# Performance work log

Hardware: AMD Instinct MI355X
Metric: run time of the kernel (lower is better)

## Reference

```python
import jax, jax.numpy as jnp
import numpy as np

DETA = 0.2  # constant margin scale (args.deta_const == True)
N = 33554432


def setup_inputs() -> dict:
    key = jax.random.key(0)
    k1, k2 = jax.random.split(key)
    y_pred = jax.random.normal(k1, (N,), dtype=jnp.float32)
    labels = jax.random.randint(k2, (N,), 0, 2, dtype=jnp.int32)
    return {"y_pred": y_pred, "labels": labels}


def reference(y_pred, labels):
    # Flattened ranking loss: deta * sum_{i in neg, j in pos} (neg_i - pos_j) / (pos_num * neg_num)
    # Algebraically: pos_num * sum(neg) - neg_num * sum(pos), avoiding the O(P*N) pairwise matrix.
    y = y_pred.reshape(-1)
    lab = labels.reshape(-1).astype(y.dtype)
    n_total = jnp.asarray(y.shape[0], dtype=y.dtype)
    pos_num = jnp.sum(lab)
    neg_num = n_total - pos_num
    sum_all = jnp.sum(y)
    sum_pos = jnp.sum(y * lab)
    sum_neg = sum_all - sum_pos
    valid = (pos_num > 0) & (neg_num > 0)
    denom = jnp.where(valid, pos_num * neg_num, jnp.ones_like(pos_num))
    loss = DETA * (pos_num * sum_neg - neg_num * sum_pos) / denom
    return jnp.where(valid, loss, jnp.zeros_like(loss))
```

## Files before the change

kernel.cpp:

```cpp
#include <hip/hip_runtime.h>


#define NBLK 2048

__global__ void aux_loss_reduce(const float* __restrict__ y,
                                const int* __restrict__ lab,
                                double* __restrict__ part, int n) {
    const int n4 = n >> 2;
    const float4* __restrict__ y4 = (const float4*)y;
    const int4* __restrict__ l4 = (const int4*)lab;

    double s_all = 0.0, s_pos = 0.0;
    int cnt = 0;

    const int idx = blockIdx.x * blockDim.x + threadIdx.x;
    const int stride = gridDim.x * blockDim.x;

    int i = idx;
    for (; i + stride < n4; i += 2 * stride) {
        float4 va = y4[i];
        int4 la = l4[i];
        float4 vb = y4[i + stride];
        int4 lb = l4[i + stride];

        s_all += (double)va.x + (double)va.y + (double)va.z + (double)va.w;
        s_pos += (la.x ? (double)va.x : 0.0) + (la.y ? (double)va.y : 0.0)
               + (la.z ? (double)va.z : 0.0) + (la.w ? (double)va.w : 0.0);
        cnt += la.x + la.y + la.z + la.w;

        s_all += (double)vb.x + (double)vb.y + (double)vb.z + (double)vb.w;
        s_pos += (lb.x ? (double)vb.x : 0.0) + (lb.y ? (double)vb.y : 0.0)
               + (lb.z ? (double)vb.z : 0.0) + (lb.w ? (double)vb.w : 0.0);
        cnt += lb.x + lb.y + lb.z + lb.w;
    }
    for (; i < n4; i += stride) {
        float4 v = y4[i];
        int4 l = l4[i];
        s_all += (double)v.x + (double)v.y + (double)v.z + (double)v.w;
        s_pos += (l.x ? (double)v.x : 0.0) + (l.y ? (double)v.y : 0.0)
               + (l.z ? (double)v.z : 0.0) + (l.w ? (double)v.w : 0.0);
        cnt += l.x + l.y + l.z + l.w;
    }
    for (int j = (n4 << 2) + idx; j < n; j += stride) {
        float v = y[j];
        int l = lab[j];
        s_all += (double)v;
        if (l) { s_pos += (double)v; cnt += l; }
    }

    double c = (double)cnt;

    for (int off = 32; off > 0; off >>= 1) {
        s_all += __shfl_down(s_all, off);
        s_pos += __shfl_down(s_pos, off);
        c     += __shfl_down(c, off);
    }

    __shared__ double sh_all[4], sh_pos[4], sh_cnt[4];
    const int wave = threadIdx.x >> 6;
    const int lane = threadIdx.x & 63;
    if (lane == 0) { sh_all[wave] = s_all; sh_pos[wave] = s_pos; sh_cnt[wave] = c; }
    __syncthreads();

    if (threadIdx.x == 0) {
        double a = 0.0, p = 0.0, cc = 0.0;
        for (int w = 0; w < 4; ++w) { a += sh_all[w]; p += sh_pos[w]; cc += sh_cnt[w]; }
        part[blockIdx.x]            = a;
        part[NBLK + blockIdx.x]     = p;
        part[2 * NBLK + blockIdx.x] = cc;
    }
}

__global__ void aux_loss_stage2(const double* __restrict__ part,
                                float* __restrict__ out, double n_total) {
    double a = 0.0, p = 0.0, cc = 0.0;
    for (int i = threadIdx.x; i < NBLK; i += blockDim.x) {
        a  += part[i];
        p  += part[NBLK + i];
        cc += part[2 * NBLK + i];
    }
    for (int off = 32; off > 0; off >>= 1) {
        a  += __shfl_down(a, off);
        p  += __shfl_down(p, off);
        cc += __shfl_down(cc, off);
    }
    __shared__ double sh_a[4], sh_p[4], sh_c[4];
    const int wave = threadIdx.x >> 6;
    const int lane = threadIdx.x & 63;
    if (lane == 0) { sh_a[wave] = a; sh_p[wave] = p; sh_c[wave] = cc; }
    __syncthreads();

    if (threadIdx.x == 0) {
        double sum_all = 0.0, sum_pos = 0.0, pos = 0.0;
        for (int w = 0; w < 4; ++w) { sum_all += sh_a[w]; sum_pos += sh_p[w]; pos += sh_c[w]; }
        double neg = n_total - pos;
        double sum_neg = sum_all - sum_pos;
        double loss = 0.0;
        if (pos > 0.0 && neg > 0.0) {
            loss = 0.2 * (pos * sum_neg - neg * sum_pos) / (pos * neg);
        }
        out[0] = (float)loss;
    }
}

extern "C" void kernel_launch(void* const* d_in, const int* in_sizes, int n_in,
                              void* d_out, int out_size, void* d_ws, size_t ws_size,
                              hipStream_t stream) {
    const float* y = (const float*)d_in[0];
    const int* lab = (const int*)d_in[1];
    int n = in_sizes[0];

    double* part = (double*)d_ws;

    aux_loss_reduce<<<NBLK, 256, 0, stream>>>(y, lab, part, n);
    aux_loss_stage2<<<1, 256, 0, stream>>>(part, (float*)d_out, (double)n);
}
```

Measured before the change: 274.9 us.

## Accumulate partial sums in FP32 per unrolled chunk and use contiguous per-block ranges

Each thread now sums 16 elements in float and only promotes to double once per chunk, replacing per-element double conversions and adds. The grid-stride loop becomes a contiguous per-block range with 4 independent vector loads in flight per thread, plus launch bounds. This aims to remove FP64 ALU cost that dominated the memory-bound reduction, at a small cost in accumulation precision.

```diff
diff --git a/kernel.cpp b/kernel.cpp
--- a/kernel.cpp
+++ b/kernel.cpp
@@ -2,50 +2,58 @@
 
 
 #define NBLK 2048
+#define TPB 256
+#define UNROLL 4
 
-__global__ void aux_loss_reduce(const float* __restrict__ y,
-                                const int* __restrict__ lab,
-                                double* __restrict__ part, int n) {
+__global__ __launch_bounds__(TPB, 8)
+void aux_loss_reduce(const float* __restrict__ y,
+                     const int* __restrict__ lab,
+                     double* __restrict__ part, int n) {
     const int n4 = n >> 2;
     const float4* __restrict__ y4 = (const float4*)y;
     const int4* __restrict__ l4 = (const int4*)lab;
 
+    const int chunk = (n4 + NBLK - 1) / NBLK;
+    const int base = blockIdx.x * chunk;
+    const int end = min(base + chunk, n4);
+
     double s_all = 0.0, s_pos = 0.0;
-    int cnt = 0;
+    long long cnt = 0;
 
-    const int idx = blockIdx.x * blockDim.x + threadIdx.x;
-    const int stride = gridDim.x * blockDim.x;
+    for (int i0 = base; i0 < end; i0 += TPB * UNROLL) {
+        float4 v[UNROLL];
+        int4 l[UNROLL];
+#pragma unroll
+        for (int u = 0; u < UNROLL; ++u) {
+            const int i = i0 + u * TPB + (int)threadIdx.x;
+            const bool ok = i < end;
+            v[u] = ok ? y4[i] : make_float4(0.f, 0.f, 0.f, 0.f);
+            l[u] = ok ? l4[i] : make_int4(0, 0, 0, 0);
+        }
+        float pa = 0.f, pp = 0.f;
+        int pc = 0;
+#pragma unroll
+        for (int u = 0; u < UNROLL; ++u) {
+            pa += (v[u].x + v[u].y) + (v[u].z + v[u].w);
+            const float mx = l[u].x ? v[u].x : 0.f;
+            const float my = l[u].y ? v[u].y : 0.f;
+            const float mz = l[u].z ? v[u].z : 0.f;
+            const float mw = l[u].w ? v[u].w : 0.f;
+            pp += (mx + my) + (mz + mw);
+            pc += l[u].x + l[u].y + l[u].z + l[u].w;
+        }
+        s_all += (double)pa;
+        s_pos += (double)pp;
+        cnt += pc;
+    }
 
-    int i = idx;
-    for (; i + stride < n4; i += 2 * stride) {
-        float4 va = y4[i];
-        int4 la = l4[i];
-        float4 vb = y4[i + stride];
-        int4 lb = l4[i + stride];
-
-        s_all += (double)va.x + (double)va.y + (double)va.z + (double)va.w;
-        s_pos += (la.x ? (double)va.x : 0.0) + (la.y ? (double)va.y : 0.0)
-               + (la.z ? (double)va.z : 0.0) + (la.w ? (double)va.w : 0.0);
-        cnt += la.x + la.y + la.z + la.w;
-
-        s_all += (double)vb.x + (double)vb.y + (double)vb.z + (double)vb.w;
-        s_pos += (lb.x ? (double)vb.x : 0.0) + (lb.y ? (double)vb.y : 0.0)
-               + (lb.z ? (double)vb.z : 0.0) + (lb.w ? (double)vb.w : 0.0);
-        cnt += lb.x + lb.y + lb.z + lb.w;
-    }
-    for (; i < n4; i += stride) {
-        float4 v = y4[i];
-        int4 l = l4[i];
-        s_all += (double)v.x + (double)v.y + (double)v.z + (double)v.w;
-        s_pos += (l.x ? (double)v.x : 0.0) + (l.y ? (double)v.y : 0.0)
-               + (l.z ? (double)v.z : 0.0) + (l.w ? (double)v.w : 0.0);
-        cnt += l.x + l.y + l.z + l.w;
-    }
-    for (int j = (n4 << 2) + idx; j < n; j += stride) {
-        float v = y[j];
-        int l = lab[j];
-        s_all += (double)v;
-        if (l) { s_pos += (double)v; cnt += l; }
+    if (blockIdx.x == 0) {
+        for (int j = (n4 << 2) + (int)threadIdx.x; j < n; j += TPB) {
+            const float v = y[j];
+            const int l = lab[j];
+            s_all += (double)v;
+            if (l) { s_pos += (double)v; cnt += l; }
+        }
     }
 
     double c = (double)cnt;
@@ -93,8 +101,8 @@
     if (threadIdx.x == 0) {
         double sum_all = 0.0, sum_pos = 0.0, pos = 0.0;
         for (int w = 0; w < 4; ++w) { sum_all += sh_a[w]; sum_pos += sh_p[w]; pos += sh_c[w]; }
-        double neg = n_total - pos;
-        double sum_neg = sum_all - sum_pos;
+        const double neg = n_total - pos;
+        const double sum_neg = sum_all - sum_pos;
         double loss = 0.0;
         if (pos > 0.0 && neg > 0.0) {
             loss = 0.2 * (pos * sum_neg - neg * sum_pos) / (pos * neg);
@@ -112,6 +120,6 @@
 
     double* part = (double*)d_ws;
 
-    aux_loss_reduce<<<NBLK, 256, 0, stream>>>(y, lab, part, n);
-    aux_loss_stage2<<<1, 256, 0, stream>>>(part, (float*)d_out, (double)n);
+    aux_loss_reduce<<<NBLK, TPB, 0, stream>>>(y, lab, part, n);
+    aux_loss_stage2<<<1, TPB, 0, stream>>>(part, (float*)d_out, (double)n);
 }
```

Result: slower. 283.9 us (+3.3%).
